# Kernel optimization log

Measured on AMD Instinct MI355X. Metric: run time of the kernel, lower is better.

## Reference

```python
import jax, jax.numpy as jnp
import numpy as np

VOCAB = 1024
EMBED_DIM = 64
COMMIT_COST = 0.25


def setup_inputs() -> dict:
    key = jax.random.key(0)
    k1, k2 = jax.random.split(key)
    z_e = jax.random.normal(k1, (64, 64, 32, 32), dtype=jnp.float32)
    # nn.Embedding init: uniform(-1/vocab, 1/vocab)
    embedding = jax.random.uniform(
        k2, (VOCAB, EMBED_DIM), dtype=jnp.float32,
        minval=-1.0 / VOCAB, maxval=1.0 / VOCAB)
    return {"z_e": z_e, "embedding": embedding}


def reference(z_e, embedding):
    b, d, h, w = z_e.shape
    # [B,D,H,W] -> [N,D]
    flat_z = jnp.transpose(z_e, (0, 2, 3, 1)).reshape(-1, d)
    # squared L2 distances to each code: [N, V]
    distances = (
        jnp.sum(flat_z * flat_z, axis=1, keepdims=True)
        + jnp.sum(embedding * embedding, axis=1)
        - 2.0 * flat_z @ embedding.T
    )
    flat_indices = jnp.argmin(distances, axis=1)
    indices = flat_indices.reshape(b, h, w)
    # gather codes and restore [B,D,H,W]
    z_q = embedding[flat_indices].reshape(b, h, w, d)
    z_q = jnp.transpose(z_q, (0, 3, 1, 2))
    quantization_loss = jnp.mean((z_q - jax.lax.stop_gradient(z_e)) ** 2)
    commitment_loss = jnp.mean((z_e - jax.lax.stop_gradient(z_q)) ** 2) * COMMIT_COST
    z_q_st = z_e + jax.lax.stop_gradient(z_q - z_e)
    # perplexity over codebook usage
    counts = jnp.zeros((VOCAB,), dtype=jnp.float32).at[flat_indices].add(1.0)
    avg_probs = counts / flat_indices.shape[0]
    perplexity = jnp.exp(-jnp.sum(avg_probs * jnp.log(avg_probs + 1e-10)))
    return (z_q_st, indices, quantization_loss, commitment_loss, perplexity)
```

## Files before the change

kernel.cpp:

```cpp
#include <hip/hip_runtime.h>
#include <math.h>

#define VOCAB 1024
#define ED 64
#define NROWS 65536
#define NELEM 4194304
#define MARGIN 2.0e-4f

typedef __attribute__((ext_vector_type(8))) short short8;
typedef __attribute__((ext_vector_type(4))) float f32x4;

__device__ __forceinline__ unsigned f2bf(float f) {
    unsigned u = __float_as_uint(f);
    u += 0x7fff + ((u >> 16) & 1);
    return u >> 16;
}

__device__ __forceinline__ unsigned long long packkey(float d, int c) {
    unsigned f = __float_as_uint(d);
    unsigned sd = (f & 0x80000000u) ? ~f : (f | 0x80000000u);
    return ((unsigned long long)sd << 32) | (unsigned)c;
}


__global__ void vq_prep(const float* __restrict__ emb, float* __restrict__ e2f,
                        uint4* __restrict__ FB, unsigned* __restrict__ hist) {
    const int tid = blockIdx.x * 256 + threadIdx.x;
    if (tid < 1024) hist[tid] = 0u;

    if (tid < VOCAB) {
        const float4* src = (const float4*)(emb + tid * ED);
        double s = 0.0;
        #pragma unroll
        for (int g = 0; g < 16; ++g) {
            float4 f = src[g];
            s = fma((double)f.x, (double)f.x, s);
            s = fma((double)f.y, (double)f.y, s);
            s = fma((double)f.z, (double)f.z, s);
            s = fma((double)f.w, (double)f.w, s);
        }
        e2f[tid] = (float)s;
    }
    #pragma unroll
    for (int e = 0; e < 4; ++e) {
        const int i = e * 2048 + tid;
        const int n = i & 15, q = (i >> 4) & 3, kh = (i >> 6) & 1, T = i >> 7;
        const int code = T * 16 + n;
        const int k0 = kh * 32 + q * 8;
        const float4* sp = (const float4*)(emb + code * 64 + k0);
        float4 f0 = sp[0], f1 = sp[1];
        uint4 pk;
        pk.x = f2bf(f0.x) | (f2bf(f0.y) << 16);
        pk.y = f2bf(f0.z) | (f2bf(f0.w) << 16);
        pk.z = f2bf(f1.x) | (f2bf(f1.y) << 16);
        pk.w = f2bf(f1.z) | (f2bf(f1.w) << 16);
        FB[i] = pk;
    }
}

__global__ __launch_bounds__(256, 2)
void vq_main(const float* __restrict__ z, const float* __restrict__ emb,
             const float* __restrict__ e2f, const uint4* __restrict__ FB,
             float* __restrict__ out, double* __restrict__ lossp,
             unsigned* __restrict__ hist) {
    __shared__ float e2s[1024];
    __shared__ float rowb1[64], rowb2[64], rowb3[64];
    __shared__ int   rowi1[64], rowi2[64], rowfi[64];
    __shared__ float zs[64 * 64];
    __shared__ float znsh[64];
    __shared__ int   flrows[64], frows2[64];
    __shared__ int   flcs, nfulls;
    __shared__ double wls[4];

    const int t = threadIdx.x;
    const int w = t >> 6, lane = t & 63;
    const int q = lane >> 4, n_lo = lane & 15;
    const int bk = blockIdx.x;
    const int n0 = bk * 64;
    const int b  = n0 >> 10;
    const int sb = n0 & 1023;

    #pragma unroll
    for (int i = 0; i < 4; ++i) e2s[i * 256 + t] = e2f[i * 256 + t];

    short8 af[2];
    {
        const int s = sb + w * 16 + n_lo;
        const float* zp = z + (size_t)b * 65536 + s;
        #pragma unroll
        for (int kh = 0; kh < 2; ++kh) {
            short8 fr;
            #pragma unroll
            for (int j = 0; j < 8; ++j) {
                int d = kh * 32 + q * 8 + j;
                fr[j] = (short)f2bf(-2.0f * zp[d * 1024]);
            }
            af[kh] = fr;
        }
    }

    float b1[4], b2[4], b3[4]; int i1[4], i2[4];
    #pragma unroll
    for (int sl = 0; sl < 4; ++sl) {
        b1[sl] = 3.4e38f; b2[sl] = 3.4e38f; b3[sl] = 3.4e38f;
        i1[sl] = 0; i2[sl] = 0;
    }

    __syncthreads();

    const short8* FBs = (const short8*)FB;
    #pragma unroll 4
    for (int T = 0; T < 64; ++T) {
        short8 bf0 = FBs[T * 128 + lane];
        short8 bf1 = FBs[T * 128 + 64 + lane];
        const int cb = T * 16 + n_lo;
        const float e2 = e2s[cb];
        f32x4 a; a[0] = e2; a[1] = e2; a[2] = e2; a[3] = e2;
        a = __builtin_amdgcn_mfma_f32_16x16x32_bf16(af[0], bf0, a, 0, 0, 0);
        a = __builtin_amdgcn_mfma_f32_16x16x32_bf16(af[1], bf1, a, 0, 0, 0);
        #pragma unroll
        for (int reg = 0; reg < 4; ++reg) {
            float s0 = a[reg];
            b3[reg] = __builtin_amdgcn_fmed3f(s0, b2[reg], b3[reg]);
            bool lt2 = s0 < b2[reg];
            bool lt  = s0 < b1[reg];
            i2[reg] = lt2 ? (lt ? i1[reg] : cb) : i2[reg];
            b2[reg] = __builtin_amdgcn_fmed3f(s0, b1[reg], b2[reg]);
            i1[reg] = lt ? cb : i1[reg];
            b1[reg] = lt ? s0 : b1[reg];
        }
    }

    #pragma unroll
    for (int m = 1; m < 16; m <<= 1) {
        #pragma unroll
        for (int sl = 0; sl < 4; ++sl) {
            float oa1 = __shfl_xor(b1[sl], m, 64);
            float oa2 = __shfl_xor(b2[sl], m, 64);
            float oa3 = __shfl_xor(b3[sl], m, 64);
            int   oj1 = __shfl_xor(i1[sl], m, 64);
            int   oj2 = __shfl_xor(i2[sl], m, 64);
            bool take = (oa1 < b1[sl]) || (oa1 == b1[sl] && oj1 < i1[sl]);
            float w1  = take ? oa1 : b1[sl];  int ni1 = take ? oj1 : i1[sl];
            float l1v = take ? b1[sl] : oa1;  int il1 = take ? i1[sl] : oj1;
            float wt2 = take ? oa2 : b2[sl];  int iw2 = take ? oj2 : i2[sl];
            float wt3 = take ? oa3 : b3[sl];
            float lt2v = take ? b2[sl] : oa2;
            bool t2 = wt2 < l1v;
            float nb2 = t2 ? wt2 : l1v;       int ni2 = t2 ? iw2 : il1;
            float nb3 = fminf(fmaxf(l1v, wt2), fminf(wt3, lt2v));
            b1[sl] = w1;  i1[sl] = ni1;
            b2[sl] = nb2; i2[sl] = ni2;
            b3[sl] = nb3;
        }
    }
    if (n_lo == 0) {
        #pragma unroll
        for (int reg = 0; reg < 4; ++reg) {
            int row = w * 16 + q * 4 + reg;
            rowb1[row] = b1[reg];
            rowb2[row] = b2[reg];
            rowb3[row] = b3[reg];
            rowi1[row] = i1[reg];
            rowi2[row] = i2[reg];
        }
    }
    __syncthreads();

    if (t < 64) {
        const float thr = rowb1[t] + MARGIN;
        const bool pf = rowb2[t] < thr;
        const bool ff = rowb3[t] < thr;
        unsigned long long pm = __ballot(pf);
        if (t == 0) flcs = __popcll(pm);
        if (pf) {
            const int rank = __popcll(pm & ((1ULL << t) - 1ULL));
            flrows[rank] = t | (ff ? 256 : 0);
            rowfi[t] = rank;
        }
        unsigned long long fm = __ballot(ff);
        if (t == 0) nfulls = __popcll(fm);
        if (ff) {
            const int rank = __popcll(fm & ((1ULL << t) - 1ULL));
            frows2[rank] = t;
        }
    }
    __syncthreads();
    const int flc = flcs;
    const int nfull = nfulls;

    if (flc > 0) {
        {
            const int fi = t >> 2, d0 = (t & 3) * 16;
            if (fi < flc) {
                const int r = flrows[fi] & 255;
                const float* zp = z + (size_t)b * 65536 + (size_t)d0 * 1024 + (sb + r);
                #pragma unroll
                for (int k = 0; k < 16; ++k)
                    zs[fi * 64 + d0 + k] = zp[(size_t)k * 1024];
            }
        }
        __syncthreads();
        if (t < flc) {
            const float* zp = zs + t * 64;
            double a = 0.0;
            for (int k = 0; k < 64; ++k) { const double v = (double)zp[k]; a = fma(v, v, a); }
            znsh[t] = (float)a;
        }
        __syncthreads();

        if (t < flc) {
            const int ent = flrows[t];
            if (!(ent & 256)) {
                const int r = ent & 255;
                const float zn = znsh[t];
                const int c1 = rowi1[r], c2 = rowi2[r];
                const float* zp = zs + t * 64;
                const float4* e1p = (const float4*)(emb + (size_t)c1 * 64);
                const float4* e2p = (const float4*)(emb + (size_t)c2 * 64);
                float m1 = 0.f, m2 = 0.f;
                #pragma unroll
                for (int k4 = 0; k4 < 16; ++k4) {
                    const float4 zz = *(const float4*)(zp + k4 * 4);
                    const float4 ea = e1p[k4], eb = e2p[k4];
                    m1 = fmaf(zz.x, ea.x, m1); m1 = fmaf(zz.y, ea.y, m1);
                    m1 = fmaf(zz.z, ea.z, m1); m1 = fmaf(zz.w, ea.w, m1);
                    m2 = fmaf(zz.x, eb.x, m2); m2 = fmaf(zz.y, eb.y, m2);
                    m2 = fmaf(zz.z, eb.z, m2); m2 = fmaf(zz.w, eb.w, m2);
                }
                const float t1 = zn + e2s[c1];
                const float t2v = zn + e2s[c2];
                const float d1 = t1 - 2.0f * m1;
                const float d2 = t2v - 2.0f * m2;
                const int cw = (d2 < d1 || (d2 == d1 && c2 < c1)) ? c2 : c1;
                rowi1[r] = cw;
            }
        }

        for (int fj = w; fj < nfull; fj += 4) {
            const int r = frows2[fj];
            const int fi = rowfi[r];
            const float zn = znsh[fi];
            const float4* zz4 = (const float4*)(zs + fi * 64);
            unsigned long long best = ~0ULL;
            #pragma unroll 1
            for (int j = 0; j < 16; ++j) {
                const int c = j * 64 + lane;
                const float4* ep4 = (const float4*)(emb + (size_t)c * 64);
                float m = 0.f;
                #pragma unroll
                for (int k4 = 0; k4 < 16; ++k4) {
                    const float4 e4v = ep4[k4];
                    const float4 zz = zz4[k4];
                    m = fmaf(zz.x, e4v.x, m); m = fmaf(zz.y, e4v.y, m);
                    m = fmaf(zz.z, e4v.z, m); m = fmaf(zz.w, e4v.w, m);
                }
                const float tt = zn + e2s[c];
                const float d = tt - 2.0f * m;
                const unsigned long long kk = packkey(d, c);
                if (kk < best) best = kk;
            }
            #pragma unroll
            for (int mo = 32; mo > 0; mo >>= 1) {
                unsigned long long o = __shfl_xor(best, mo, 64);
                if (o < best) best = o;
            }
            if (lane == 0) rowi1[r] = (int)(unsigned)(best & 0xffffffffu);
        }
        __syncthreads();
    }

    if (t < 64) {
        const int code = rowi1[t];
        out[NELEM + n0 + t] = (float)code;
        atomicAdd(&hist[code], 1u);
    }

    {
        const int r = lane;
        const int code2 = rowi1[r];
        const int scol = sb + r;
        double lsum = 0.0;
        #pragma unroll
        for (int i = 0; i < 4; ++i) {
            const int d4 = w * 4 + i;
            float4 e4 = *(const float4*)(emb + code2 * 64 + d4 * 4);
            float es[4] = {e4.x, e4.y, e4.z, e4.w};
            #pragma unroll
            for (int j = 0; j < 4; ++j) {
                int d = d4 * 4 + j;
                size_t off = (size_t)b * 65536 + (size_t)d * 1024 + scol;
                float zv = z[off];
                out[off] = zv + (es[j] - zv);
                double df = (double)es[j] - (double)zv;
                lsum = fma(df, df, lsum);
            }
        }
        #pragma unroll
        for (int off = 32; off > 0; off >>= 1)
            lsum += __shfl_down(lsum, off, 64);
        if (lane == 0) wls[w] = lsum;
    }
    __syncthreads();
    if (t == 0) lossp[bk] = wls[0] + wls[1] + wls[2] + wls[3];
}

__global__ void vq_finalize_kernel(const unsigned* __restrict__ hist,
                                   const double* __restrict__ lossp,
                                   float* __restrict__ out) {
    __shared__ double red[256], red2[256];
    int t = threadIdx.x;
    double ssum = 0.0, lsum = 0.0;
    for (int i = t; i < VOCAB; i += 256) {
        double p = (double)hist[i] / (double)NROWS;
        ssum += p * log(p + 1e-10);
    }
    for (int i = t; i < 1024; i += 256) lsum += lossp[i];
    red[t] = ssum; red2[t] = lsum;
    __syncthreads();
    for (int off = 128; off > 0; off >>= 1) {
        if (t < off) { red[t] += red[t + off]; red2[t] += red2[t + off]; }
        __syncthreads();
    }
    if (t == 0) {
        double qv = red2[0] / (double)NELEM;
        out[NELEM + NROWS + 0] = (float)qv;
        out[NELEM + NROWS + 1] = (float)(qv * 0.25);
        out[NELEM + NROWS + 2] = (float)exp(-red[0]);
    }
}

extern "C" void kernel_launch(void* const* d_in, const int* in_sizes, int n_in,
                              void* d_out, int out_size, void* d_ws, size_t ws_size,
                              hipStream_t stream) {
    const float* z   = (const float*)d_in[0];
    const float* emb = (const float*)d_in[1];
    float* out = (float*)d_out;

    float*    e2f   = (float*)d_ws;
    unsigned* hist  = (unsigned*)((char*)d_ws + 4096);
    uint4*    FB    = (uint4*)((char*)d_ws + 8192);
    double*   lossp = (double*)((char*)d_ws + 139264);

    vq_prep<<<dim3(8), dim3(256), 0, stream>>>(emb, e2f, FB, hist);
    vq_main<<<dim3(1024), dim3(256), 0, stream>>>(z, emb, e2f, FB, out, lossp, hist);
    vq_finalize_kernel<<<dim3(1), dim3(256), 0, stream>>>(hist, lossp, out);
}
```

Measured before the change: 154.6 us.

## Split codebook scan across two wave-groups per block and merge top-3 results

The main kernel now runs 512 threads per block instead of 256. The two halves of the block each scan half of the 1024 codes for the same 64 rows, and their top-3 candidates are merged through shared memory. The intent is to double the waves working on each row tile, shortening the serial MFMA and argmin loop per block and giving more latency hiding. In exchange, each block needs more registers and must do an extra merge step, which may reduce how many blocks fit on a CU.

Measured after the change: 208.3 us. +34.7%, slower.

```diff
diff --git a/kernel.cpp b/kernel.cpp
--- a/kernel.cpp
+++ b/kernel.cpp
@@ -58,22 +58,24 @@
     }
 }
 
-__global__ __launch_bounds__(256, 2)
+__global__ __launch_bounds__(512, 2)
 void vq_main(const float* __restrict__ z, const float* __restrict__ emb,
              const float* __restrict__ e2f, const uint4* __restrict__ FB,
              float* __restrict__ out, double* __restrict__ lossp,
              unsigned* __restrict__ hist) {
     __shared__ float e2s[1024];
-    __shared__ float rowb1[64], rowb2[64], rowb3[64];
-    __shared__ int   rowi1[64], rowi2[64], rowfi[64];
+    __shared__ float hb1[2][64], hb2[2][64], hb3[2][64];
+    __shared__ int   hi1[2][64], hi2[2][64];
+    __shared__ int   rowC[64], rowC2[64], rowfi[64];
     __shared__ float zs[64 * 64];
     __shared__ float znsh[64];
     __shared__ int   flrows[64], frows2[64];
     __shared__ int   flcs, nfulls;
-    __shared__ double wls[4];
+    __shared__ double wls[8];
 
     const int t = threadIdx.x;
     const int w = t >> 6, lane = t & 63;
+    const int half = w >> 2, wl = w & 3;
     const int q = lane >> 4, n_lo = lane & 15;
     const int bk = blockIdx.x;
     const int n0 = bk * 64;
@@ -81,11 +83,11 @@
     const int sb = n0 & 1023;
 
     #pragma unroll
-    for (int i = 0; i < 4; ++i) e2s[i * 256 + t] = e2f[i * 256 + t];
+    for (int i = 0; i < 2; ++i) e2s[i * 512 + t] = e2f[i * 512 + t];
 
     short8 af[2];
     {
-        const int s = sb + w * 16 + n_lo;
+        const int s = sb + wl * 16 + n_lo;
         const float* zp = z + (size_t)b * 65536 + s;
         #pragma unroll
         for (int kh = 0; kh < 2; ++kh) {
@@ -110,7 +112,8 @@
 
     const short8* FBs = (const short8*)FB;
     #pragma unroll 4
-    for (int T = 0; T < 64; ++T) {
+    for (int tt = 0; tt < 32; ++tt) {
+        const int T = half * 32 + tt;
         short8 bf0 = FBs[T * 128 + lane];
         short8 bf1 = FBs[T * 128 + 64 + lane];
         const int cb = T * 16 + n_lo;
@@ -157,20 +160,36 @@
     if (n_lo == 0) {
         #pragma unroll
         for (int reg = 0; reg < 4; ++reg) {
-            int row = w * 16 + q * 4 + reg;
-            rowb1[row] = b1[reg];
-            rowb2[row] = b2[reg];
-            rowb3[row] = b3[reg];
-            rowi1[row] = i1[reg];
-            rowi2[row] = i2[reg];
+            int row = wl * 16 + q * 4 + reg;
+            hb1[half][row] = b1[reg];
+            hb2[half][row] = b2[reg];
+            hb3[half][row] = b3[reg];
+            hi1[half][row] = i1[reg];
+            hi2[half][row] = i2[reg];
         }
     }
     __syncthreads();
 
     if (t < 64) {
-        const float thr = rowb1[t] + MARGIN;
-        const bool pf = rowb2[t] < thr;
-        const bool ff = rowb3[t] < thr;
+        float a1 = hb1[0][t], a2v = hb2[0][t], a3 = hb3[0][t];
+        int   j1 = hi1[0][t], j2 = hi2[0][t];
+        float oa1 = hb1[1][t], oa2 = hb2[1][t], oa3 = hb3[1][t];
+        int   oj1 = hi1[1][t], oj2 = hi2[1][t];
+        bool take = (oa1 < a1) || (oa1 == a1 && oj1 < j1);
+        float w1  = take ? oa1 : a1;   int ni1 = take ? oj1 : j1;
+        float l1v = take ? a1 : oa1;   int il1 = take ? j1 : oj1;
+        float wt2 = take ? oa2 : a2v;  int iw2 = take ? oj2 : j2;
+        float wt3 = take ? oa3 : a3;
+        float lt2v = take ? a2v : oa2;
+        bool t2 = wt2 < l1v;
+        float nb2 = t2 ? wt2 : l1v;    int ni2 = t2 ? iw2 : il1;
+        float nb3 = fminf(fmaxf(l1v, wt2), fminf(wt3, lt2v));
+        rowC[t]  = ni1;
+        rowC2[t] = ni2;
+
+        const float thr = w1 + MARGIN;
+        const bool pf = nb2 < thr;
+        const bool ff = nb3 < thr;
         unsigned long long pm = __ballot(pf);
         if (t == 0) flcs = __popcll(pm);
         if (pf) {
@@ -191,12 +210,12 @@
 
     if (flc > 0) {
         {
-            const int fi = t >> 2, d0 = (t & 3) * 16;
+            const int fi = t >> 3, d0 = (t & 7) * 8;
             if (fi < flc) {
                 const int r = flrows[fi] & 255;
                 const float* zp = z + (size_t)b * 65536 + (size_t)d0 * 1024 + (sb + r);
                 #pragma unroll
-                for (int k = 0; k < 16; ++k)
+                for (int k = 0; k < 8; ++k)
                     zs[fi * 64 + d0 + k] = zp[(size_t)k * 1024];
             }
         }
@@ -214,7 +233,7 @@
             if (!(ent & 256)) {
                 const int r = ent & 255;
                 const float zn = znsh[t];
-                const int c1 = rowi1[r], c2 = rowi2[r];
+                const int c1 = rowC[r], c2 = rowC2[r];
                 const float* zp = zs + t * 64;
                 const float4* e1p = (const float4*)(emb + (size_t)c1 * 64);
                 const float4* e2p = (const float4*)(emb + (size_t)c2 * 64);
@@ -233,11 +252,11 @@
                 const float d1 = t1 - 2.0f * m1;
                 const float d2 = t2v - 2.0f * m2;
                 const int cw = (d2 < d1 || (d2 == d1 && c2 < c1)) ? c2 : c1;
-                rowi1[r] = cw;
-            }
-        }
-
-        for (int fj = w; fj < nfull; fj += 4) {
+                rowC[r] = cw;
+            }
+        }
+
+        for (int fj = w; fj < nfull; fj += 8) {
             const int r = frows2[fj];
             const int fi = rowfi[r];
             const float zn = znsh[fi];
@@ -265,25 +284,25 @@
                 unsigned long long o = __shfl_xor(best, mo, 64);
                 if (o < best) best = o;
             }
-            if (lane == 0) rowi1[r] = (int)(unsigned)(best & 0xffffffffu);
+            if (lane == 0) rowC[r] = (int)(unsigned)(best & 0xffffffffu);
         }
         __syncthreads();
     }
 
     if (t < 64) {
-        const int code = rowi1[t];
+        const int code = rowC[t];
         out[NELEM + n0 + t] = (float)code;
         atomicAdd(&hist[code], 1u);
     }
 
     {
         const int r = lane;
-        const int code2 = rowi1[r];
+        const int code2 = rowC[r];
         const int scol = sb + r;
         double lsum = 0.0;
         #pragma unroll
-        for (int i = 0; i < 4; ++i) {
-            const int d4 = w * 4 + i;
+        for (int i = 0; i < 2; ++i) {
+            const int d4 = w * 2 + i;
             float4 e4 = *(const float4*)(emb + code2 * 64 + d4 * 4);
             float es[4] = {e4.x, e4.y, e4.z, e4.w};
             #pragma unroll
@@ -302,7 +321,12 @@
         if (lane == 0) wls[w] = lsum;
     }
     __syncthreads();
-    if (t == 0) lossp[bk] = wls[0] + wls[1] + wls[2] + wls[3];
+    if (t == 0) {
+        double s = 0.0;
+        #pragma unroll
+        for (int i = 0; i < 8; ++i) s += wls[i];
+        lossp[bk] = s;
+    }
 }
 
 __global__ void vq_finalize_kernel(const unsigned* __restrict__ hist,
@@ -343,6 +367,6 @@
     double*   lossp = (double*)((char*)d_ws + 139264);
 
     vq_prep<<<dim3(8), dim3(256), 0, stream>>>(emb, e2f, FB, hist);
-    vq_main<<<dim3(1024), dim3(256), 0, stream>>>(z, emb, e2f, FB, out, lossp, hist);
+    vq_main<<<dim3(1024), dim3(512), 0, stream>>>(z, emb, e2f, FB, out, lossp, hist);
     vq_finalize_kernel<<<dim3(1), dim3(256), 0, stream>>>(hist, lossp, out);
 }
```

## Process 128 rows per block to reuse codebook fragments across two row tiles

Applied to the files above, without the earlier changes.

Each block now handles 128 rows instead of 64, and every wave computes two 16-row MFMA tiles against each loaded codebook fragment. Each bf16 codebook load is therefore used twice, halving codebook traffic per row and the number of blocks. The ballot-based compaction of fallback rows becomes a two-wave scan, and the gather/store phase is regrouped to match. In exchange it uses more registers and LDS per block and launches only 512 blocks, which may lower occupancy on 256 CUs.

Measured after the change: 180.8 us. 1.17x slower.

```diff
diff --git a/kernel.cpp b/kernel.cpp
--- a/kernel.cpp
+++ b/kernel.cpp
@@ -64,11 +64,12 @@
              float* __restrict__ out, double* __restrict__ lossp,
              unsigned* __restrict__ hist) {
     __shared__ float e2s[1024];
-    __shared__ float rowb1[64], rowb2[64], rowb3[64];
-    __shared__ int   rowi1[64], rowi2[64], rowfi[64];
-    __shared__ float zs[64 * 64];
-    __shared__ float znsh[64];
-    __shared__ int   flrows[64], frows2[64];
+    __shared__ float rowb1[128], rowb2[128], rowb3[128];
+    __shared__ int   rowi1[128], rowi2[128], rowfi[128];
+    __shared__ float zs[128 * 64];
+    __shared__ float znsh[128];
+    __shared__ int   flrows[128], frows2[128];
+    __shared__ int   wcp[2], wcf[2];
     __shared__ int   flcs, nfulls;
     __shared__ double wls[4];
 
@@ -76,16 +77,17 @@
     const int w = t >> 6, lane = t & 63;
     const int q = lane >> 4, n_lo = lane & 15;
     const int bk = blockIdx.x;
-    const int n0 = bk * 64;
+    const int n0 = bk * 128;
     const int b  = n0 >> 10;
     const int sb = n0 & 1023;
 
     #pragma unroll
     for (int i = 0; i < 4; ++i) e2s[i * 256 + t] = e2f[i * 256 + t];
 
-    short8 af[2];
-    {
-        const int s = sb + w * 16 + n_lo;
+    short8 af[2][2];
+    #pragma unroll
+    for (int rt = 0; rt < 2; ++rt) {
+        const int s = sb + w * 32 + rt * 16 + n_lo;
         const float* zp = z + (size_t)b * 65536 + s;
         #pragma unroll
         for (int kh = 0; kh < 2; ++kh) {
@@ -95,13 +97,13 @@
                 int d = kh * 32 + q * 8 + j;
                 fr[j] = (short)f2bf(-2.0f * zp[d * 1024]);
             }
-            af[kh] = fr;
-        }
-    }
-
-    float b1[4], b2[4], b3[4]; int i1[4], i2[4];
-    #pragma unroll
-    for (int sl = 0; sl < 4; ++sl) {
+            af[rt][kh] = fr;
+        }
+    }
+
+    float b1[8], b2[8], b3[8]; int i1[8], i2[8];
+    #pragma unroll
+    for (int sl = 0; sl < 8; ++sl) {
         b1[sl] = 3.4e38f; b2[sl] = 3.4e38f; b3[sl] = 3.4e38f;
         i1[sl] = 0; i2[sl] = 0;
     }
@@ -115,26 +117,30 @@
         short8 bf1 = FBs[T * 128 + 64 + lane];
         const int cb = T * 16 + n_lo;
         const float e2 = e2s[cb];
-        f32x4 a; a[0] = e2; a[1] = e2; a[2] = e2; a[3] = e2;
-        a = __builtin_amdgcn_mfma_f32_16x16x32_bf16(af[0], bf0, a, 0, 0, 0);
-        a = __builtin_amdgcn_mfma_f32_16x16x32_bf16(af[1], bf1, a, 0, 0, 0);
-        #pragma unroll
-        for (int reg = 0; reg < 4; ++reg) {
-            float s0 = a[reg];
-            b3[reg] = __builtin_amdgcn_fmed3f(s0, b2[reg], b3[reg]);
-            bool lt2 = s0 < b2[reg];
-            bool lt  = s0 < b1[reg];
-            i2[reg] = lt2 ? (lt ? i1[reg] : cb) : i2[reg];
-            b2[reg] = __builtin_amdgcn_fmed3f(s0, b1[reg], b2[reg]);
-            i1[reg] = lt ? cb : i1[reg];
-            b1[reg] = lt ? s0 : b1[reg];
+        #pragma unroll
+        for (int rt = 0; rt < 2; ++rt) {
+            f32x4 a; a[0] = e2; a[1] = e2; a[2] = e2; a[3] = e2;
+            a = __builtin_amdgcn_mfma_f32_16x16x32_bf16(af[rt][0], bf0, a, 0, 0, 0);
+            a = __builtin_amdgcn_mfma_f32_16x16x32_bf16(af[rt][1], bf1, a, 0, 0, 0);
+            #pragma unroll
+            for (int reg = 0; reg < 4; ++reg) {
+                const int sl = rt * 4 + reg;
+                float s0 = a[reg];
+                b3[sl] = __builtin_amdgcn_fmed3f(s0, b2[sl], b3[sl]);
+                bool lt2 = s0 < b2[sl];
+                bool lt  = s0 < b1[sl];
+                i2[sl] = lt2 ? (lt ? i1[sl] : cb) : i2[sl];
+                b2[sl] = __builtin_amdgcn_fmed3f(s0, b1[sl], b2[sl]);
+                i1[sl] = lt ? cb : i1[sl];
+                b1[sl] = lt ? s0 : b1[sl];
+            }
         }
     }
 
     #pragma unroll
     for (int m = 1; m < 16; m <<= 1) {
         #pragma unroll
-        for (int sl = 0; sl < 4; ++sl) {
+        for (int sl = 0; sl < 8; ++sl) {
             float oa1 = __shfl_xor(b1[sl], m, 64);
             float oa2 = __shfl_xor(b2[sl], m, 64);
             float oa3 = __shfl_xor(b3[sl], m, 64);
@@ -156,47 +162,58 @@
     }
     if (n_lo == 0) {
         #pragma unroll
-        for (int reg = 0; reg < 4; ++reg) {
-            int row = w * 16 + q * 4 + reg;
-            rowb1[row] = b1[reg];
-            rowb2[row] = b2[reg];
-            rowb3[row] = b3[reg];
-            rowi1[row] = i1[reg];
-            rowi2[row] = i2[reg];
-        }
-    }
-    __syncthreads();
-
-    if (t < 64) {
+        for (int rt = 0; rt < 2; ++rt) {
+            #pragma unroll
+            for (int reg = 0; reg < 4; ++reg) {
+                const int sl = rt * 4 + reg;
+                const int row = w * 32 + rt * 16 + q * 4 + reg;
+                rowb1[row] = b1[sl];
+                rowb2[row] = b2[sl];
+                rowb3[row] = b3[sl];
+                rowi1[row] = i1[sl];
+                rowi2[row] = i2[sl];
+            }
+        }
+    }
+    __syncthreads();
+
+    unsigned long long pm = 0, fm = 0;
+    bool pf = false, ff = false;
+    if (t < 128) {
         const float thr = rowb1[t] + MARGIN;
-        const bool pf = rowb2[t] < thr;
-        const bool ff = rowb3[t] < thr;
-        unsigned long long pm = __ballot(pf);
-        if (t == 0) flcs = __popcll(pm);
+        pf = rowb2[t] < thr;
+        ff = rowb3[t] < thr;
+        pm = __ballot(pf);
+        fm = __ballot(ff);
+        if (lane == 0) { wcp[w] = __popcll(pm); wcf[w] = __popcll(fm); }
+    }
+    __syncthreads();
+    if (t < 128) {
+        const int basep = (w == 1) ? wcp[0] : 0;
+        const int basef = (w == 1) ? wcf[0] : 0;
         if (pf) {
-            const int rank = __popcll(pm & ((1ULL << t) - 1ULL));
+            const int rank = basep + __popcll(pm & ((1ULL << lane) - 1ULL));
             flrows[rank] = t | (ff ? 256 : 0);
             rowfi[t] = rank;
         }
-        unsigned long long fm = __ballot(ff);
-        if (t == 0) nfulls = __popcll(fm);
         if (ff) {
-            const int rank = __popcll(fm & ((1ULL << t) - 1ULL));
-            frows2[rank] = t;
-        }
-    }
+            const int rankf = basef + __popcll(fm & ((1ULL << lane) - 1ULL));
+            frows2[rankf] = t;
+        }
+    }
+    if (t == 0) { flcs = wcp[0] + wcp[1]; nfulls = wcf[0] + wcf[1]; }
     __syncthreads();
     const int flc = flcs;
     const int nfull = nfulls;
 
     if (flc > 0) {
         {
-            const int fi = t >> 2, d0 = (t & 3) * 16;
+            const int fi = t >> 1, d0 = (t & 1) * 32;
             if (fi < flc) {
                 const int r = flrows[fi] & 255;
                 const float* zp = z + (size_t)b * 65536 + (size_t)d0 * 1024 + (sb + r);
                 #pragma unroll
-                for (int k = 0; k < 16; ++k)
+                for (int k = 0; k < 32; ++k)
                     zs[fi * 64 + d0 + k] = zp[(size_t)k * 1024];
             }
         }
@@ -270,20 +287,20 @@
         __syncthreads();
     }
 
-    if (t < 64) {
+    if (t < 128) {
         const int code = rowi1[t];
         out[NELEM + n0 + t] = (float)code;
         atomicAdd(&hist[code], 1u);
     }
 
     {
-        const int r = lane;
+        const int r = t & 127, tg = t >> 7;
         const int code2 = rowi1[r];
         const int scol = sb + r;
         double lsum = 0.0;
         #pragma unroll
-        for (int i = 0; i < 4; ++i) {
-            const int d4 = w * 4 + i;
+        for (int i = 0; i < 8; ++i) {
+            const int d4 = tg * 8 + i;
             float4 e4 = *(const float4*)(emb + code2 * 64 + d4 * 4);
             float es[4] = {e4.x, e4.y, e4.z, e4.w};
             #pragma unroll
@@ -315,7 +332,7 @@
         double p = (double)hist[i] / (double)NROWS;
         ssum += p * log(p + 1e-10);
     }
-    for (int i = t; i < 1024; i += 256) lsum += lossp[i];
+    for (int i = t; i < 512; i += 256) lsum += lossp[i];
     red[t] = ssum; red2[t] = lsum;
     __syncthreads();
     for (int off = 128; off > 0; off >>= 1) {
@@ -343,6 +360,6 @@
     double*   lossp = (double*)((char*)d_ws + 139264);
 
     vq_prep<<<dim3(8), dim3(256), 0, stream>>>(emb, e2f, FB, hist);
-    vq_main<<<dim3(1024), dim3(256), 0, stream>>>(z, emb, e2f, FB, out, lossp, hist);
+    vq_main<<<dim3(512), dim3(256), 0, stream>>>(z, emb, e2f, FB, out, lossp, hist);
     vq_finalize_kernel<<<dim3(1), dim3(256), 0, stream>>>(hist, lossp, out);
 }
```
